# Kernel tuning notes

Measured on AMD Instinct MI355X. Metric: run time of the kernel, lower is better.

The kernel has to match this reference:

```python
import jax, jax.numpy as jnp
import numpy as np

B, T, D, H = 2, 2048, 1024, 16
HD = D // H

def setup_inputs() -> dict:
    key = jax.random.key(0)
    ks = jax.random.split(key, 5)
    fan = D
    bound_w = float(np.sqrt(6.0 / fan))  # kaiming_uniform-ish scale
    return {
        "x": jax.random.normal(ks[0], (B, T, D), dtype=jnp.float32),
        "W_qkv": jax.random.uniform(ks[1], (3 * D, D), minval=-bound_w, maxval=bound_w, dtype=jnp.float32),
        "b_qkv": jax.random.uniform(ks[2], (3 * D,), minval=-bound_w, maxval=bound_w, dtype=jnp.float32),
        "W_proj": jax.random.uniform(ks[3], (D, D), minval=-bound_w, maxval=bound_w, dtype=jnp.float32),
        "b_proj": jax.random.uniform(ks[4], (D,), minval=-bound_w, maxval=bound_w, dtype=jnp.float32),
    }

def reference(x, W_qkv, b_qkv, W_proj, b_proj):
    Bx, Tx, C = x.shape
    h, hd = H, C // H
    qkv = x @ W_qkv.T + b_qkv                      # (B,T,3C)
    q, k, v = jnp.split(qkv, 3, axis=-1)
    # (B,T,C) -> (B,h,T,hd)
    q = q.reshape(Bx, Tx, h, hd).transpose(0, 2, 1, 3)
    k = k.reshape(Bx, Tx, h, hd).transpose(0, 2, 1, 3)
    v = v.reshape(Bx, Tx, h, hd).transpose(0, 2, 1, 3)
    scale = hd ** -0.5
    scores = jnp.einsum('bhqd,bhkd->bhqk', q, k) * scale
    causal = jnp.tril(jnp.ones((Tx, Tx), dtype=bool))
    scores = jnp.where(causal, scores, -jnp.inf)
    weights = jax.nn.softmax(scores, axis=-1)      # stable softmax, same math
    out = jnp.einsum('bhqk,bhkd->bhqd', weights, v)
    out = out.transpose(0, 2, 1, 3).reshape(Bx, Tx, C)
    return out @ W_proj.T + b_proj
```

## Files before the change

### kernel.cpp

```cpp
#include <hip/hip_runtime.h>

typedef unsigned short u16;
typedef __attribute__((ext_vector_type(8))) short bf16x8;
typedef __attribute__((ext_vector_type(4))) short bf16x4;
typedef __attribute__((ext_vector_type(4))) float f32x4;

#define Bb 2
#define Tt 2048
#define Dd 1024
#define Hh 16
#define HD 64
#define NTOK (Bb*Tt)
#define QKVN (3*Dd)

__device__ __forceinline__ u16 f2b(float f) {
    unsigned u = __float_as_uint(f);
    unsigned r = (u + 0x7fffu + ((u >> 16) & 1u)) >> 16;
    return (u16)r;
}

__device__ __forceinline__ void g2l16(const u16* g, u16* l) {
    __builtin_amdgcn_global_load_lds(
        (const __attribute__((address_space(1))) unsigned int*)g,
        (__attribute__((address_space(3))) unsigned int*)l,
        16, 0, 0);
}

__device__ __forceinline__ unsigned pk2(float lo, float hi) {
    return __builtin_amdgcn_perm(__float_as_uint(hi), __float_as_uint(lo), 0x07060302u);
}

#define N4X  (NTOK * Dd / 4)
#define N4WQ (3 * Dd * Dd / 4)
#define N4WP (Dd * Dd / 4)
__global__ void cvt_all(const float* __restrict__ x, const float* __restrict__ wq,
                        const float* __restrict__ wp, u16* __restrict__ xb,
                        u16* __restrict__ wqb, u16* __restrict__ wpb) {
    int i = blockIdx.x * blockDim.x + threadIdx.x;
    const float* src; u16* dst; int j;
    if (i < N4X)                { src = x;  dst = xb;  j = i; }
    else if (i < N4X + N4WQ)    { src = wq; dst = wqb; j = i - N4X; }
    else                        { src = wp; dst = wpb; j = i - N4X - N4WQ; }
    float4 f = ((const float4*)src)[j];
    ushort4 o;
    o.x = f2b(f.x); o.y = f2b(f.y); o.z = f2b(f.z); o.w = f2b(f.w);
    ((ushort4*)dst)[j] = o;
}

#define TRS 136

__global__ __launch_bounds__(256, 3)
void gemm_qkv(const u16* __restrict__ A, const u16* __restrict__ Bt,
              const float* __restrict__ bias,
              u16* __restrict__ C16, u16* __restrict__ Vt) {
    const int N = QKVN, K = Dd;
    __shared__ alignas(16) u16 smem[128 * TRS];
    u16* As = smem;
    u16* Bs = smem + 8192;
    const int tid = threadIdx.x;
    const int wave = tid >> 6, lane = tid & 63;
    const int quad = lane >> 4, l16 = lane & 15;
    const int wm = (wave & 1) * 64, wn = (wave >> 1) * 64;
    const int m0 = blockIdx.x * 128, n0 = blockIdx.y * 128;
    const int lrow = lane >> 2, lcol = (lane & 3) << 3;

    f32x4 acc[4][4];
#pragma unroll
    for (int i = 0; i < 4; ++i)
#pragma unroll
        for (int j = 0; j < 4; ++j)
            acc[i][j] = (f32x4){0.f, 0.f, 0.f, 0.f};

    for (int k0 = 0; k0 < K; k0 += 64) {
#pragma unroll
        for (int h = 0; h < 2; ++h)
#pragma unroll
            for (int c = 0; c < 2; ++c) {
                const int rb = (c * 4 + wave) * 16;
                g2l16(A  + (size_t)(m0 + rb + lrow) * K + k0 + h * 32 + lcol,
                      &As[h * 4096 + rb * 32 + (lane << 3)]);
                g2l16(Bt + (size_t)(n0 + rb + lrow) * K + k0 + h * 32 + lcol,
                      &Bs[h * 4096 + rb * 32 + (lane << 3)]);
            }
        __syncthreads();
        bf16x8 a[4][2], b[4][2];
#pragma unroll
        for (int h = 0; h < 2; ++h) {
#pragma unroll
            for (int i = 0; i < 4; ++i)
                a[i][h] = *(const bf16x8*)(&As[h * 4096 + (wm + i * 16 + l16) * 32 + quad * 8]);
#pragma unroll
            for (int i = 0; i < 4; ++i)
                b[i][h] = *(const bf16x8*)(&Bs[h * 4096 + (wn + i * 16 + l16) * 32 + quad * 8]);
        }
#pragma unroll
        for (int h = 0; h < 2; ++h)
#pragma unroll
            for (int i = 0; i < 4; ++i)
#pragma unroll
                for (int j = 0; j < 4; ++j)
                    acc[i][j] = __builtin_amdgcn_mfma_f32_16x16x32_bf16(a[i][h], b[j][h], acc[i][j], 0, 0, 0);
        __syncthreads();
    }

    float b4[4];
#pragma unroll
    for (int j = 0; j < 4; ++j) b4[j] = bias[n0 + wn + j * 16 + l16];
    const bool isV = (n0 >= 2 * Dd);

    if (!isV) {
#pragma unroll
        for (int i = 0; i < 4; ++i)
#pragma unroll
            for (int j = 0; j < 4; ++j)
#pragma unroll
                for (int r = 0; r < 4; ++r) {
                    int m = m0 + wm + i * 16 + quad * 4 + r;
                    int n = n0 + wn + j * 16 + l16;
                    C16[(size_t)m * N + n] = f2b(acc[i][j][r] + b4[j]);
                }
    } else {
#pragma unroll
        for (int i = 0; i < 4; ++i)
#pragma unroll
            for (int j = 0; j < 4; ++j)
#pragma unroll
                for (int r = 0; r < 4; ++r) {
                    int ml = wm + i * 16 + quad * 4 + r;
                    int nl = wn + j * 16 + l16;
                    smem[nl * TRS + ml] = f2b(acc[i][j][r] + b4[j]);
                }
        __syncthreads();
        const int bidx = m0 >> 11, t0 = m0 & 2047;
        const int nl = tid >> 1, toff = (tid & 1) * 64;
        u16* dst = Vt + (size_t)bidx * (Hh * HD * Tt)
                      + (size_t)(n0 - 2 * Dd + nl) * Tt + t0 + toff;
        const u16* srcl = &smem[nl * TRS + toff];
#pragma unroll
        for (int k = 0; k < 8; ++k)
            *(uint4*)(dst + k * 8) = *(const uint4*)(srcl + k * 8);
    }
}

__global__ __launch_bounds__(256, 2)
void gemm_proj(const u16* __restrict__ A, const u16* __restrict__ Bt,
               const float* __restrict__ bias, float* __restrict__ Co) {
    const int N = Dd, K = Dd;
    __shared__ alignas(16) u16 As[2 * 128 * 32];
    __shared__ alignas(16) u16 Bs[2 * 64 * 32];
    const int tid = threadIdx.x;
    const int wave = tid >> 6, lane = tid & 63;
    const int quad = lane >> 4, l16 = lane & 15;
    const int wm = (wave & 1) * 64, wn = (wave >> 1) * 32;
    const int m0 = blockIdx.x * 128, n0 = blockIdx.y * 64;
    const int lrow = lane >> 2, lcol = (lane & 3) << 3;

    f32x4 acc[4][2];
#pragma unroll
    for (int i = 0; i < 4; ++i)
#pragma unroll
        for (int j = 0; j < 2; ++j)
            acc[i][j] = (f32x4){0.f, 0.f, 0.f, 0.f};

    for (int k0 = 0; k0 < K; k0 += 64) {
#pragma unroll
        for (int h = 0; h < 2; ++h) {
#pragma unroll
            for (int c = 0; c < 2; ++c) {
                const int rb = (c * 4 + wave) * 16;
                g2l16(A + (size_t)(m0 + rb + lrow) * K + k0 + h * 32 + lcol,
                      &As[h * 4096 + rb * 32 + (lane << 3)]);
            }
            g2l16(Bt + (size_t)(n0 + wave * 16 + lrow) * K + k0 + h * 32 + lcol,
                  &Bs[h * 2048 + (wave * 16) * 32 + (lane << 3)]);
        }
        __syncthreads();
        bf16x8 a[4][2], b[2][2];
#pragma unroll
        for (int h = 0; h < 2; ++h) {
#pragma unroll
            for (int i = 0; i < 4; ++i)
                a[i][h] = *(const bf16x8*)(&As[h * 4096 + (wm + i * 16 + l16) * 32 + quad * 8]);
#pragma unroll
            for (int j = 0; j < 2; ++j)
                b[j][h] = *(const bf16x8*)(&Bs[h * 2048 + (wn + j * 16 + l16) * 32 + quad * 8]);
        }
#pragma unroll
        for (int h = 0; h < 2; ++h)
#pragma unroll
            for (int i = 0; i < 4; ++i)
#pragma unroll
                for (int j = 0; j < 2; ++j)
                    acc[i][j] = __builtin_amdgcn_mfma_f32_16x16x32_bf16(a[i][h], b[j][h], acc[i][j], 0, 0, 0);
        __syncthreads();
    }

    float b2[2];
#pragma unroll
    for (int j = 0; j < 2; ++j) b2[j] = bias[n0 + wn + j * 16 + l16];

#pragma unroll
    for (int i = 0; i < 4; ++i)
#pragma unroll
        for (int j = 0; j < 2; ++j)
#pragma unroll
            for (int r = 0; r < 4; ++r) {
                int m = m0 + wm + i * 16 + quad * 4 + r;
                int n = n0 + wn + j * 16 + l16;
                Co[(size_t)m * N + n] = acc[i][j][r] + b2[j];
            }
}

#define LKP 80
#define FMX 24.0f

__global__ __launch_bounds__(256, 3)
void attn_fwd(const u16* __restrict__ qkv, const u16* __restrict__ Vt,
              u16* __restrict__ Ao) {
    const int bid = blockIdx.x;
    const int xcd = bid & 7, li = bid >> 3;
    const int bh = (xcd << 2) | (li >> 4);
    const int pair = li & 15;
    const int hh = bh & (Hh - 1), bidx = bh >> 4;
    const u16* Qp = qkv + (size_t)bidx * Tt * QKVN + hh * HD;
    const u16* Kp = Qp + Dd;
    const u16* Vp = Vt + (size_t)bh * HD * Tt;
    const int tid = threadIdx.x;
    const int wave = tid >> 6, lane = tid & 63;
    const int quad = lane >> 4, l16 = lane & 15;

    __shared__ alignas(16) u16 Ks[2][64 * LKP];
    __shared__ alignas(16) u16 Vs[2][64 * LKP];

    const int srow = tid >> 3, scol = (tid & 7) << 3;
    const int st0 = srow * LKP + scol, st1 = (srow + 32) * LKP + scol;
    const int svw = ((srow >> 2) & 3) << 3;
    const int sv0 = srow * LKP + (scol ^ svw);
    const int sv1 = (srow + 32) * LKP + (scol ^ svw);
    const float sc = 0.125f * 1.44269504f;

    const int vswz = ((l16 >> 2) & 3) << 3;
    int vcoff[4];
#pragma unroll
    for (int nt = 0; nt < 4; ++nt)
        vcoff[nt] = (nt * 16 + quad * 4) ^ vswz;

    float mb[16];
#pragma unroll
    for (int nt = 0; nt < 4; ++nt)
#pragma unroll
        for (int r = 0; r < 4; ++r)
            mb[nt * 4 + r] = (nt * 16 + quad * 4 + r <= wave * 16 + l16) ? -FMX : -250.0f;

    for (int half = 0; half < 2; ++half) {
        const int qt = half ? pair : (31 - pair);
        const int qrow_g = qt * 64 + wave * 16 + l16;
        bf16x8 aq[2];
#pragma unroll
        for (int kk = 0; kk < 2; ++kk)
            aq[kk] = *(const bf16x8*)(Qp + (size_t)qrow_g * QKVN + kk * 32 + quad * 8);

        f32x4 o[4];
#pragma unroll
        for (int nt = 0; nt < 4; ++nt) o[nt] = (f32x4){0.f, 0.f, 0.f, 0.f};
        float lsum = 0.f;

        {
            uint4 k0r = *(const uint4*)(Kp + (size_t)srow * QKVN + scol);
            uint4 k1r = *(const uint4*)(Kp + (size_t)(srow + 32) * QKVN + scol);
            uint4 v0r = *(const uint4*)(Vp + (size_t)srow * Tt + scol);
            uint4 v1r = *(const uint4*)(Vp + (size_t)(srow + 32) * Tt + scol);
            *(uint4*)(&Ks[0][st0]) = k0r;
            *(uint4*)(&Ks[0][st1]) = k1r;
            *(uint4*)(&Vs[0][sv0]) = v0r;
            *(uint4*)(&Vs[0][sv1]) = v1r;
        }
        __syncthreads();

        const u16* kp0 = Kp + (size_t)(64 + srow) * QKVN + scol;
        const u16* kp1 = kp0 + (size_t)32 * QKVN;
        const u16* vp0 = Vp + (size_t)srow * Tt + 64 + scol;
        const u16* vp1 = vp0 + (size_t)32 * Tt;

        u16* Kcur = &Ks[0][0]; u16* Knxt = &Ks[1][0];
        u16* Vcur = &Vs[0][0]; u16* Vnxt = &Vs[1][0];

        for (int kt = 0; kt < qt; ++kt) {
            uint4 k0r = *(const uint4*)kp0;
            uint4 k1r = *(const uint4*)kp1;
            uint4 v0r = *(const uint4*)vp0;
            uint4 v1r = *(const uint4*)vp1;
            kp0 += (size_t)64 * QKVN; kp1 += (size_t)64 * QKVN;
            vp0 += 64; vp1 += 64;

            f32x4 s[4];
#pragma unroll
            for (int nt = 0; nt < 4; ++nt) {
                f32x4 z = (f32x4){0.f, 0.f, 0.f, 0.f};
#pragma unroll
                for (int kk = 0; kk < 2; ++kk) {
                    bf16x8 ak = *(const bf16x8*)(&Kcur[(nt * 16 + l16) * LKP + kk * 32 + quad * 8]);
                    z = __builtin_amdgcn_mfma_f32_16x16x32_bf16(ak, aq[kk], z, 0, 0, 0);
                }
                s[nt] = z;
            }

#pragma unroll
            for (int nt = 0; nt < 4; ++nt)
#pragma unroll
                for (int r = 0; r < 4; ++r) {
                    float p = exp2f(__builtin_fmaf(s[nt][r], sc, -FMX));
                    s[nt][r] = p;
                    lsum += p;
                }

            bf16x4 ps[4];
#pragma unroll
            for (int nt = 0; nt < 4; ++nt) {
                uint2 w;
                w.x = pk2(s[nt][0], s[nt][1]);
                w.y = pk2(s[nt][2], s[nt][3]);
                ps[nt] = *(bf16x4*)&w;
            }

#pragma unroll
            for (int nt = 0; nt < 4; ++nt)
#pragma unroll
                for (int ntO = 0; ntO < 4; ++ntO) {
                    bf16x4 av = *(const bf16x4*)(&Vcur[(ntO * 16 + l16) * LKP + vcoff[nt]]);
                    o[ntO] = __builtin_amdgcn_mfma_f32_16x16x16bf16_1k(av, ps[nt], o[ntO], 0, 0, 0);
                }

            *(uint4*)(&Knxt[st0]) = k0r;
            *(uint4*)(&Knxt[st1]) = k1r;
            *(uint4*)(&Vnxt[sv0]) = v0r;
            *(uint4*)(&Vnxt[sv1]) = v1r;
            u16* t;
            t = Kcur; Kcur = Knxt; Knxt = t;
            t = Vcur; Vcur = Vnxt; Vnxt = t;
            __syncthreads();
        }

        {
            f32x4 s[4];
#pragma unroll
            for (int nt = 0; nt < 4; ++nt) {
                f32x4 z = (f32x4){0.f, 0.f, 0.f, 0.f};
#pragma unroll
                for (int kk = 0; kk < 2; ++kk) {
                    bf16x8 ak = *(const bf16x8*)(&Kcur[(nt * 16 + l16) * LKP + kk * 32 + quad * 8]);
                    z = __builtin_amdgcn_mfma_f32_16x16x32_bf16(ak, aq[kk], z, 0, 0, 0);
                }
                s[nt] = z;
            }
#pragma unroll
            for (int nt = 0; nt < 4; ++nt)
#pragma unroll
                for (int r = 0; r < 4; ++r) {
                    float p = exp2f(__builtin_fmaf(s[nt][r], sc, mb[nt * 4 + r]));
                    s[nt][r] = p;
                    lsum += p;
                }
            bf16x4 ps[4];
#pragma unroll
            for (int nt = 0; nt < 4; ++nt) {
                uint2 w;
                w.x = pk2(s[nt][0], s[nt][1]);
                w.y = pk2(s[nt][2], s[nt][3]);
                ps[nt] = *(bf16x4*)&w;
            }
#pragma unroll
            for (int nt = 0; nt < 4; ++nt)
#pragma unroll
                for (int ntO = 0; ntO < 4; ++ntO) {
                    bf16x4 av = *(const bf16x4*)(&Vcur[(ntO * 16 + l16) * LKP + vcoff[nt]]);
                    o[ntO] = __builtin_amdgcn_mfma_f32_16x16x16bf16_1k(av, ps[nt], o[ntO], 0, 0, 0);
                }
        }
        __syncthreads();

        lsum += __shfl_xor(lsum, 16, 64);
        lsum += __shfl_xor(lsum, 32, 64);
        const float rinv = 1.0f / lsum;
        u16* orow = Ao + ((size_t)bidx * Tt + qrow_g) * Dd + hh * HD;
#pragma unroll
        for (int nt = 0; nt < 4; ++nt) {
            ushort4 p4;
            p4.x = f2b(o[nt][0] * rinv); p4.y = f2b(o[nt][1] * rinv);
            p4.z = f2b(o[nt][2] * rinv); p4.w = f2b(o[nt][3] * rinv);
            *(ushort4*)(orow + nt * 16 + quad * 4) = p4;
        }
    }
}

extern "C" void kernel_launch(void* const* d_in, const int* in_sizes, int n_in,
                              void* d_out, int out_size, void* d_ws, size_t ws_size,
                              hipStream_t stream) {
    const float* x      = (const float*)d_in[0];
    const float* W_qkv  = (const float*)d_in[1];
    const float* b_qkv  = (const float*)d_in[2];
    const float* W_proj = (const float*)d_in[3];
    const float* b_proj = (const float*)d_in[4];
    float* out = (float*)d_out;

    char* ws = (char*)d_ws;
    u16* Wprojb = (u16*)(ws);
    u16* Wqkvb  = (u16*)(ws + (2u << 20));
    u16* xb     = (u16*)(ws + (8u << 20));
    u16* qkvb   = (u16*)(ws + (16u << 20));
    u16* Vtb    = (u16*)(ws + (40u << 20));
    u16* attnb  = (u16*)(ws + (2u << 20));

    cvt_all<<<(N4X + N4WQ + N4WP) / 256, 256, 0, stream>>>(x, W_qkv, W_proj, xb, Wqkvb, Wprojb);

    {
        dim3 grid(NTOK / 128, QKVN / 128);
        gemm_qkv<<<grid, 256, 0, stream>>>(xb, Wqkvb, b_qkv, qkvb, Vtb);
    }
    {
        attn_fwd<<<dim3(512), 256, 0, stream>>>(qkvb, Vtb, attnb);
    }
    {
        dim3 grid(NTOK / 128, Dd / 64);
        gemm_proj<<<grid, 256, 0, stream>>>(attnb, Wprojb, b_proj, out);
    }
}
```

Measured before the change: 174.9 us.

## Process both causal query tiles in one K/V sweep to share loads

Measured after the change: 180.0 us. 1.03x slower.

```diff
diff --git a/kernel.cpp b/kernel.cpp
--- a/kernel.cpp
+++ b/kernel.cpp
@@ -234,16 +234,17 @@
 
     const int srow = tid >> 3, scol = (tid & 7) << 3;
     const int st0 = srow * LKP + scol, st1 = (srow + 32) * LKP + scol;
-    const int svw = ((srow >> 2) & 3) << 3;
-    const int sv0 = srow * LKP + (scol ^ svw);
-    const int sv1 = (srow + 32) * LKP + (scol ^ svw);
+    const int swz = ((srow >> 2) & 3) << 2;
+    const int sv0 = srow * LKP + (scol ^ (swz & 8));
+    const int sv1 = (srow + 32) * LKP + (scol ^ (swz & 8));
+    const bool vswap = (swz & 4) != 0;
     const float sc = 0.125f * 1.44269504f;
 
-    const int vswz = ((l16 >> 2) & 3) << 3;
+    const int rswz = ((l16 >> 2) & 3) << 2;
     int vcoff[4];
 #pragma unroll
     for (int nt = 0; nt < 4; ++nt)
-        vcoff[nt] = (nt * 16 + quad * 4) ^ vswz;
+        vcoff[nt] = (nt * 16 + quad * 4) ^ rswz;
 
     float mb[16];
 #pragma unroll
@@ -252,47 +253,96 @@
         for (int r = 0; r < 4; ++r)
             mb[nt * 4 + r] = (nt * 16 + quad * 4 + r <= wave * 16 + l16) ? -FMX : -250.0f;
 
-    for (int half = 0; half < 2; ++half) {
-        const int qt = half ? pair : (31 - pair);
-        const int qrow_g = qt * 64 + wave * 16 + l16;
-        bf16x8 aq[2];
-#pragma unroll
-        for (int kk = 0; kk < 2; ++kk)
-            aq[kk] = *(const bf16x8*)(Qp + (size_t)qrow_g * QKVN + kk * 32 + quad * 8);
-
-        f32x4 o[4];
-#pragma unroll
-        for (int nt = 0; nt < 4; ++nt) o[nt] = (f32x4){0.f, 0.f, 0.f, 0.f};
-        float lsum = 0.f;
-
-        {
-            uint4 k0r = *(const uint4*)(Kp + (size_t)srow * QKVN + scol);
-            uint4 k1r = *(const uint4*)(Kp + (size_t)(srow + 32) * QKVN + scol);
-            uint4 v0r = *(const uint4*)(Vp + (size_t)srow * Tt + scol);
-            uint4 v1r = *(const uint4*)(Vp + (size_t)(srow + 32) * Tt + scol);
-            *(uint4*)(&Ks[0][st0]) = k0r;
-            *(uint4*)(&Ks[0][st1]) = k1r;
-            *(uint4*)(&Vs[0][sv0]) = v0r;
-            *(uint4*)(&Vs[0][sv1]) = v1r;
-        }
-        __syncthreads();
-
-        const u16* kp0 = Kp + (size_t)(64 + srow) * QKVN + scol;
-        const u16* kp1 = kp0 + (size_t)32 * QKVN;
-        const u16* vp0 = Vp + (size_t)srow * Tt + 64 + scol;
-        const u16* vp1 = vp0 + (size_t)32 * Tt;
-
-        u16* Kcur = &Ks[0][0]; u16* Knxt = &Ks[1][0];
-        u16* Vcur = &Vs[0][0]; u16* Vnxt = &Vs[1][0];
-
-        for (int kt = 0; kt < qt; ++kt) {
-            uint4 k0r = *(const uint4*)kp0;
-            uint4 k1r = *(const uint4*)kp1;
-            uint4 v0r = *(const uint4*)vp0;
-            uint4 v1r = *(const uint4*)vp1;
-            kp0 += (size_t)64 * QKVN; kp1 += (size_t)64 * QKVN;
-            vp0 += 64; vp1 += 64;
-
+    const int qtA = 31 - pair, qtB = pair;
+    const int qrowA = qtA * 64 + wave * 16 + l16;
+    const int qrowB = qtB * 64 + wave * 16 + l16;
+    bf16x8 aqA[2], aqB[2];
+#pragma unroll
+    for (int kk = 0; kk < 2; ++kk) {
+        aqA[kk] = *(const bf16x8*)(Qp + (size_t)qrowA * QKVN + kk * 32 + quad * 8);
+        aqB[kk] = *(const bf16x8*)(Qp + (size_t)qrowB * QKVN + kk * 32 + quad * 8);
+    }
+
+    f32x4 oA[4], oB[4];
+#pragma unroll
+    for (int nt = 0; nt < 4; ++nt) {
+        oA[nt] = (f32x4){0.f, 0.f, 0.f, 0.f};
+        oB[nt] = (f32x4){0.f, 0.f, 0.f, 0.f};
+    }
+    float lsA = 0.f, lsB = 0.f;
+
+    {
+        uint4 k0r = *(const uint4*)(Kp + (size_t)srow * QKVN + scol);
+        uint4 k1r = *(const uint4*)(Kp + (size_t)(srow + 32) * QKVN + scol);
+        uint4 v0r = *(const uint4*)(Vp + (size_t)srow * Tt + scol);
+        uint4 v1r = *(const uint4*)(Vp + (size_t)(srow + 32) * Tt + scol);
+        *(uint4*)(&Ks[0][st0]) = k0r;
+        *(uint4*)(&Ks[0][st1]) = k1r;
+        uint4 v0s = vswap ? (uint4){v0r.z, v0r.w, v0r.x, v0r.y} : v0r;
+        uint4 v1s = vswap ? (uint4){v1r.z, v1r.w, v1r.x, v1r.y} : v1r;
+        *(uint4*)(&Vs[0][sv0]) = v0s;
+        *(uint4*)(&Vs[0][sv1]) = v1s;
+    }
+    __syncthreads();
+
+    const u16* kp0 = Kp + (size_t)(64 + srow) * QKVN + scol;
+    const u16* kp1 = kp0 + (size_t)32 * QKVN;
+    const u16* vp0 = Vp + (size_t)srow * Tt + 64 + scol;
+    const u16* vp1 = vp0 + (size_t)32 * Tt;
+
+    u16* Kcur = &Ks[0][0]; u16* Knxt = &Ks[1][0];
+    u16* Vcur = &Vs[0][0]; u16* Vnxt = &Vs[1][0];
+
+    for (int kt = 0; kt < qtA; ++kt) {
+        uint4 k0r = *(const uint4*)kp0;
+        uint4 k1r = *(const uint4*)kp1;
+        uint4 v0r = *(const uint4*)vp0;
+        uint4 v1r = *(const uint4*)vp1;
+        kp0 += (size_t)64 * QKVN; kp1 += (size_t)64 * QKVN;
+        vp0 += 64; vp1 += 64;
+
+        if (kt <= qtB) {
+            const bool dg = (kt == qtB);
+            f32x4 sA[4], sB[4];
+#pragma unroll
+            for (int nt = 0; nt < 4; ++nt) {
+                f32x4 zA = (f32x4){0.f, 0.f, 0.f, 0.f};
+                f32x4 zB = (f32x4){0.f, 0.f, 0.f, 0.f};
+#pragma unroll
+                for (int kk = 0; kk < 2; ++kk) {
+                    bf16x8 ak = *(const bf16x8*)(&Kcur[(nt * 16 + l16) * LKP + kk * 32 + quad * 8]);
+                    zA = __builtin_amdgcn_mfma_f32_16x16x32_bf16(ak, aqA[kk], zA, 0, 0, 0);
+                    zB = __builtin_amdgcn_mfma_f32_16x16x32_bf16(ak, aqB[kk], zB, 0, 0, 0);
+                }
+                sA[nt] = zA; sB[nt] = zB;
+            }
+#pragma unroll
+            for (int nt = 0; nt < 4; ++nt)
+#pragma unroll
+                for (int r = 0; r < 4; ++r) {
+                    float pA = exp2f(__builtin_fmaf(sA[nt][r], sc, -FMX));
+                    float bb = dg ? mb[nt * 4 + r] : -FMX;
+                    float pB = exp2f(__builtin_fmaf(sB[nt][r], sc, bb));
+                    sA[nt][r] = pA; lsA += pA;
+                    sB[nt][r] = pB; lsB += pB;
+                }
+            bf16x4 psA[4], psB[4];
+#pragma unroll
+            for (int nt = 0; nt < 4; ++nt) {
+                uint2 wA, wB;
+                wA.x = pk2(sA[nt][0], sA[nt][1]); wA.y = pk2(sA[nt][2], sA[nt][3]);
+                wB.x = pk2(sB[nt][0], sB[nt][1]); wB.y = pk2(sB[nt][2], sB[nt][3]);
+                psA[nt] = *(bf16x4*)&wA; psB[nt] = *(bf16x4*)&wB;
+            }
+#pragma unroll
+            for (int nt = 0; nt < 4; ++nt)
+#pragma unroll
+                for (int ntO = 0; ntO < 4; ++ntO) {
+                    bf16x4 av = *(const bf16x4*)(&Vcur[(ntO * 16 + l16) * LKP + vcoff[nt]]);
+                    oA[ntO] = __builtin_amdgcn_mfma_f32_16x16x16bf16_1k(av, psA[nt], oA[ntO], 0, 0, 0);
+                    oB[ntO] = __builtin_amdgcn_mfma_f32_16x16x16bf16_1k(av, psB[nt], oB[ntO], 0, 0, 0);
+                }
+        } else {
             f32x4 s[4];
 #pragma unroll
             for (int nt = 0; nt < 4; ++nt) {
@@ -300,20 +350,18 @@
 #pragma unroll
                 for (int kk = 0; kk < 2; ++kk) {
                     bf16x8 ak = *(const bf16x8*)(&Kcur[(nt * 16 + l16) * LKP + kk * 32 + quad * 8]);
-                    z = __builtin_amdgcn_mfma_f32_16x16x32_bf16(ak, aq[kk], z, 0, 0, 0);
+                    z = __builtin_amdgcn_mfma_f32_16x16x32_bf16(ak, aqA[kk], z, 0, 0, 0);
                 }
                 s[nt] = z;
             }
-
 #pragma unroll
             for (int nt = 0; nt < 4; ++nt)
 #pragma unroll
                 for (int r = 0; r < 4; ++r) {
                     float p = exp2f(__builtin_fmaf(s[nt][r], sc, -FMX));
                     s[nt][r] = p;
-                    lsum += p;
-                }
-
+                    lsA += p;
+                }
             bf16x4 ps[4];
 #pragma unroll
             for (int nt = 0; nt < 4; ++nt) {
@@ -322,74 +370,80 @@
                 w.y = pk2(s[nt][2], s[nt][3]);
                 ps[nt] = *(bf16x4*)&w;
             }
-
 #pragma unroll
             for (int nt = 0; nt < 4; ++nt)
 #pragma unroll
                 for (int ntO = 0; ntO < 4; ++ntO) {
                     bf16x4 av = *(const bf16x4*)(&Vcur[(ntO * 16 + l16) * LKP + vcoff[nt]]);
-                    o[ntO] = __builtin_amdgcn_mfma_f32_16x16x16bf16_1k(av, ps[nt], o[ntO], 0, 0, 0);
-                }
-
-            *(uint4*)(&Knxt[st0]) = k0r;
-            *(uint4*)(&Knxt[st1]) = k1r;
-            *(uint4*)(&Vnxt[sv0]) = v0r;
-            *(uint4*)(&Vnxt[sv1]) = v1r;
-            u16* t;
-            t = Kcur; Kcur = Knxt; Knxt = t;
-            t = Vcur; Vcur = Vnxt; Vnxt = t;
-            __syncthreads();
-        }
-
-        {
-            f32x4 s[4];
-#pragma unroll
-            for (int nt = 0; nt < 4; ++nt) {
-                f32x4 z = (f32x4){0.f, 0.f, 0.f, 0.f};
-#pragma unroll
-                for (int kk = 0; kk < 2; ++kk) {
-                    bf16x8 ak = *(const bf16x8*)(&Kcur[(nt * 16 + l16) * LKP + kk * 32 + quad * 8]);
-                    z = __builtin_amdgcn_mfma_f32_16x16x32_bf16(ak, aq[kk], z, 0, 0, 0);
-                }
-                s[nt] = z;
-            }
-#pragma unroll
-            for (int nt = 0; nt < 4; ++nt)
-#pragma unroll
-                for (int r = 0; r < 4; ++r) {
-                    float p = exp2f(__builtin_fmaf(s[nt][r], sc, mb[nt * 4 + r]));
-                    s[nt][r] = p;
-                    lsum += p;
-                }
-            bf16x4 ps[4];
-#pragma unroll
-            for (int nt = 0; nt < 4; ++nt) {
-                uint2 w;
-                w.x = pk2(s[nt][0], s[nt][1]);
-                w.y = pk2(s[nt][2], s[nt][3]);
-                ps[nt] = *(bf16x4*)&w;
-            }
-#pragma unroll
-            for (int nt = 0; nt < 4; ++nt)
-#pragma unroll
-                for (int ntO = 0; ntO < 4; ++ntO) {
-                    bf16x4 av = *(const bf16x4*)(&Vcur[(ntO * 16 + l16) * LKP + vcoff[nt]]);
-                    o[ntO] = __builtin_amdgcn_mfma_f32_16x16x16bf16_1k(av, ps[nt], o[ntO], 0, 0, 0);
-                }
-        }
-        __syncthreads();
-
-        lsum += __shfl_xor(lsum, 16, 64);
-        lsum += __shfl_xor(lsum, 32, 64);
-        const float rinv = 1.0f / lsum;
-        u16* orow = Ao + ((size_t)bidx * Tt + qrow_g) * Dd + hh * HD;
+                    oA[ntO] = __builtin_amdgcn_mfma_f32_16x16x16bf16_1k(av, ps[nt], oA[ntO], 0, 0, 0);
+                }
+        }
+
+        *(uint4*)(&Knxt[st0]) = k0r;
+        *(uint4*)(&Knxt[st1]) = k1r;
+        uint4 v0s = vswap ? (uint4){v0r.z, v0r.w, v0r.x, v0r.y} : v0r;
+        uint4 v1s = vswap ? (uint4){v1r.z, v1r.w, v1r.x, v1r.y} : v1r;
+        *(uint4*)(&Vnxt[sv0]) = v0s;
+        *(uint4*)(&Vnxt[sv1]) = v1s;
+        u16* t;
+        t = Kcur; Kcur = Knxt; Knxt = t;
+        t = Vcur; Vcur = Vnxt; Vnxt = t;
+        __syncthreads();
+    }
+
+    {
+        f32x4 s[4];
 #pragma unroll
         for (int nt = 0; nt < 4; ++nt) {
-            ushort4 p4;
-            p4.x = f2b(o[nt][0] * rinv); p4.y = f2b(o[nt][1] * rinv);
-            p4.z = f2b(o[nt][2] * rinv); p4.w = f2b(o[nt][3] * rinv);
-            *(ushort4*)(orow + nt * 16 + quad * 4) = p4;
-        }
+            f32x4 z = (f32x4){0.f, 0.f, 0.f, 0.f};
+#pragma unroll
+            for (int kk = 0; kk < 2; ++kk) {
+                bf16x8 ak = *(const bf16x8*)(&Kcur[(nt * 16 + l16) * LKP + kk * 32 + quad * 8]);
+                z = __builtin_amdgcn_mfma_f32_16x16x32_bf16(ak, aqA[kk], z, 0, 0, 0);
+            }
+            s[nt] = z;
+        }
+#pragma unroll
+        for (int nt = 0; nt < 4; ++nt)
+#pragma unroll
+            for (int r = 0; r < 4; ++r) {
+                float p = exp2f(__builtin_fmaf(s[nt][r], sc, mb[nt * 4 + r]));
+                s[nt][r] = p;
+                lsA += p;
+            }
+        bf16x4 ps[4];
+#pragma unroll
+        for (int nt = 0; nt < 4; ++nt) {
+            uint2 w;
+            w.x = pk2(s[nt][0], s[nt][1]);
+            w.y = pk2(s[nt][2], s[nt][3]);
+            ps[nt] = *(bf16x4*)&w;
+        }
+#pragma unroll
+        for (int nt = 0; nt < 4; ++nt)
+#pragma unroll
+            for (int ntO = 0; ntO < 4; ++ntO) {
+                bf16x4 av = *(const bf16x4*)(&Vcur[(ntO * 16 + l16) * LKP + vcoff[nt]]);
+                oA[ntO] = __builtin_amdgcn_mfma_f32_16x16x16bf16_1k(av, ps[nt], oA[ntO], 0, 0, 0);
+            }
+    }
+
+    lsA += __shfl_xor(lsA, 16, 64);
+    lsA += __shfl_xor(lsA, 32, 64);
+    lsB += __shfl_xor(lsB, 16, 64);
+    lsB += __shfl_xor(lsB, 32, 64);
+    const float rA = 1.0f / lsA, rB = 1.0f / lsB;
+    u16* orowA = Ao + ((size_t)bidx * Tt + qrowA) * Dd + hh * HD;
+    u16* orowB = Ao + ((size_t)bidx * Tt + qrowB) * Dd + hh * HD;
+#pragma unroll
+    for (int nt = 0; nt < 4; ++nt) {
+        ushort4 pA, pB;
+        pA.x = f2b(oA[nt][0] * rA); pA.y = f2b(oA[nt][1] * rA);
+        pA.z = f2b(oA[nt][2] * rA); pA.w = f2b(oA[nt][3] * rA);
+        pB.x = f2b(oB[nt][0] * rB); pB.y = f2b(oB[nt][1] * rB);
+        pB.z = f2b(oB[nt][2] * rB); pB.w = f2b(oB[nt][3] * rB);
+        *(ushort4*)(orowA + nt * 16 + quad * 4) = pA;
+        *(ushort4*)(orowB + nt * 16 + quad * 4) = pB;
     }
 }
 
```
